# Optimization experiments

Hardware: AMD Instinct MI355X
Metric: run time of the kernel (lower is better)

Reference implementation:

```python
import jax, jax.numpy as jnp
import numpy as np

Ng, Np, B, T = 4096, 512, 128, 100

def setup_inputs() -> dict:
    key = jax.random.key(0)
    ks = jax.random.split(key, 6)
    # xavier-ish scaling for the learned weights
    def xavier(k, shape):
        fan_in, fan_out = shape[1], shape[0]
        lim = jnp.sqrt(6.0 / (fan_in + fan_out))
        return jax.random.uniform(k, shape, jnp.float32, -lim, lim)
    return {
        "v": jax.random.normal(ks[0], (B, T, 2), jnp.float32),
        "p0": jax.random.uniform(ks[1], (B, Np), jnp.float32),
        "W_enc": xavier(ks[2], (Ng, Np)),   # init_position_encoder.weight
        "W_ih": xavier(ks[3], (Ng, 2)),     # RNN weight_ih_l0
        "W_hh": xavier(ks[4], (Ng, Ng)),    # RNN weight_hh_l0
        "W_dec": xavier(ks[5], (Np, Ng)),   # decoder.weight
    }

def reference(v, p0, W_enc, W_ih, W_hh, W_dec):
    # h0 = init_position_encoder(p0): (B, Ng)
    h0 = p0 @ W_enc.T
    # precompute input projections for all steps: (T, B, Ng)
    vin = jnp.einsum('btk,gk->tbg', v, W_ih)

    def step(h, x):
        h_new = jax.nn.relu(x + h @ W_hh.T)  # (B, Ng)
        return h_new, h_new

    _, hs = jax.lax.scan(step, h0, vin)      # hs: (T, B, Ng)
    g = jnp.swapaxes(hs, 0, 1)               # (B, T, Ng)
    preds = g @ W_dec.T                      # (B, T, Np)
    return jax.nn.log_softmax(preds, axis=-1)
```

## Files before the change

### kernel.cpp

```cpp
#include <hip/hip_runtime.h>

#define NG 4096
#define NP 512
#define BSZ 128
#define NT 100

typedef _Float16 f16;
typedef __attribute__((ext_vector_type(8))) _Float16 half8;
typedef __attribute__((ext_vector_type(4))) _Float16 half4v;
typedef __attribute__((ext_vector_type(16))) float f32x16;

__device__ inline f32x16 mfma16(half8 a, half8 b, f32x16 c) {
  return __builtin_amdgcn_mfma_f32_32x32x16_f16(a, b, c, 0, 0, 0);
}
__device__ __forceinline__ void gload16(const void* g, void* l) {
  __builtin_amdgcn_global_load_lds(
      (const __attribute__((address_space(1))) void*)g,
      (__attribute__((address_space(3))) void*)l, 16, 0, 0);
}

__global__ __launch_bounds__(256) void conv_all(
    const float* __restrict__ whh, const float* __restrict__ wdec,
    const float* __restrict__ wenc, const float* __restrict__ p0,
    f16* __restrict__ whh16, f16* __restrict__ wdec16,
    f16* __restrict__ wenc16, f16* __restrict__ p016)
{
  int i = blockIdx.x * 256 + threadIdx.x;
  const float* src; f16* dst; int off;
  if (i < 4194304)      { src = whh;  dst = whh16;  off = 0; }
  else if (i < 4718592) { src = wdec; dst = wdec16; off = 4194304; }
  else if (i < 5242880) { src = wenc; dst = wenc16; off = 4718592; }
  else if (i < 5259264) { src = p0;   dst = p016;   off = 5242880; }
  else return;
  const int j = i - off;
  const float4 x = ((const float4*)src)[j];
  half4v h = { (f16)x.x, (f16)x.y, (f16)x.z, (f16)x.w };
  *(half4v*)&dst[(size_t)j * 4] = h;
}

template<int NS, int KROW>
__global__ __launch_bounds__(256, 2) void gemm_ksplit(
    const f16* __restrict__ bmat, const f16* __restrict__ amat,
    f16* __restrict__ part)
{
  constexpr int NCH = KROW / (NS * 64);
  __shared__ __align__(128) char lds[2 * 32768];
  const int tid = threadIdx.x;
  const int w = tid >> 6, lane = tid & 63;
  const int wm = w & 1, wn = w >> 1;
  const int l31 = lane & 31, hi = lane >> 5;
  const int n0 = blockIdx.y * 128;
  const int k0 = blockIdx.x * (KROW / NS);
  constexpr size_t krb = (size_t)KROW * 2;

  const int lrow8 = lane >> 3;
  const int swz = ((lane & 7) ^ lrow8) * 16;
  const char* gA = (const char*)amat;
  const char* gB = (const char*)bmat + (size_t)n0 * krb;

  f32x16 acc[2][2] = {};

  auto stage = [&](int buf, int c) {
    const size_t kb = (size_t)((k0 + c * 64) * 2) + swz;
    char* lb = lds + buf * 32768;
    #pragma unroll
    for (int j = 0; j < 4; ++j) {
      const int r = w * 32 + j * 8;
      gload16(gA + (size_t)(r + lrow8) * krb + kb, lb + r * 128);
      gload16(gB + (size_t)(r + lrow8) * krb + kb, lb + 16384 + r * 128);
    }
  };
  auto compute = [&](int buf) {
    const char* bA = lds + buf * 32768;
    const char* bB = bA + 16384;
    const int swr = (lane & 7) << 4;
    #pragma unroll
    for (int kk = 0; kk < 4; ++kk) {
      const int bc = (kk * 32 + (hi << 4)) ^ swr;
      half8 a0 = *(const half8*)(bA + (wm * 64 + l31) * 128 + bc);
      half8 a1 = *(const half8*)(bA + (wm * 64 + 32 + l31) * 128 + bc);
      half8 b0 = *(const half8*)(bB + (wn * 64 + l31) * 128 + bc);
      half8 b1 = *(const half8*)(bB + (wn * 64 + 32 + l31) * 128 + bc);
      acc[0][0] = mfma16(a0, b0, acc[0][0]);
      acc[0][1] = mfma16(a0, b1, acc[0][1]);
      acc[1][0] = mfma16(a1, b0, acc[1][0]);
      acc[1][1] = mfma16(a1, b1, acc[1][1]);
    }
  };

  stage(0, 0);
  __syncthreads();
  #pragma unroll 1
  for (int c = 0; c < NCH; ++c) {
    if (c + 1 < NCH) stage((c + 1) & 1, c + 1);
    compute(c & 1);
    __syncthreads();
  }

  f16* po = part + (size_t)blockIdx.x * (BSZ * NG);
  #pragma unroll
  for (int mf = 0; mf < 2; ++mf) {
    #pragma unroll
    for (int q = 0; q < 16; ++q) {
      const int row = wm * 64 + mf * 32 + (q & 3) + 8 * (q >> 2) + 4 * hi;
      #pragma unroll
      for (int nf = 0; nf < 2; ++nf) {
        const int col = n0 + wn * 64 + nf * 32 + l31;
        po[(size_t)row * NG + col] = (f16)acc[mf][nf][q];
      }
    }
  }
}

template<int NS, int DOBIAS>
__global__ __launch_bounds__(256) void reduce_kernel(
    const f16* __restrict__ part, const float* __restrict__ v,
    const float* __restrict__ wih, f16* __restrict__ hout, int t)
{
  const int i = blockIdx.x * 256 + threadIdx.x;
  const int b = i >> 9;
  const int gi = (i & 511) * 8;
  const half8* p = (const half8*)part + (((size_t)b * NG + gi) >> 3);
  float s[8];
  half8 q0 = p[0];
  #pragma unroll
  for (int j = 0; j < 8; ++j) s[j] = (float)q0[j];
  #pragma unroll
  for (int k = 1; k < NS; ++k) {
    half8 q = p[(size_t)k * (BSZ * NG / 8)];
    #pragma unroll
    for (int j = 0; j < 8; ++j) s[j] += (float)q[j];
  }
  half8 h;
  if (DOBIAS) {
    const float2 vb = *(const float2*)&v[((size_t)b * NT + t) * 2];
    const float4* wr = (const float4*)(wih + (size_t)gi * 2);
    #pragma unroll
    for (int j2 = 0; j2 < 4; ++j2) {
      const float4 ww = wr[j2];
      h[j2 * 2]     = (f16)fmaxf(s[j2 * 2]     + vb.x * ww.x + vb.y * ww.y, 0.f);
      h[j2 * 2 + 1] = (f16)fmaxf(s[j2 * 2 + 1] + vb.x * ww.z + vb.y * ww.w, 0.f);
    }
  } else {
    #pragma unroll
    for (int j = 0; j < 8; ++j) h[j] = (f16)s[j];
  }
  *(half8*)&hout[(size_t)b * NG + gi] = h;
}

__global__ __launch_bounds__(512, 2) void decode_kernel(
    const f16* __restrict__ hs, const f16* __restrict__ wdec16,
    float* __restrict__ out)
{
  __shared__ __align__(128) char lds[2 * 73728];
  __shared__ float redm[8][64];
  __shared__ float reds[8][64];
  __shared__ float gLS[64];
  const int tid = threadIdx.x;
  const int w = tid >> 6, lane = tid & 63;
  const int l31 = lane & 31, hi = lane >> 5;
  const int r0 = blockIdx.x * 64;

  const int lrow8 = lane >> 3;
  const int swz = ((lane & 7) ^ lrow8) * 16;
  const char* gA = (const char*)(hs + (size_t)r0 * NG);
  const char* gB = (const char*)wdec16;

  f32x16 acc[2][2] = {};

  auto stage = [&](int buf, int c) {
    const size_t kb = (size_t)(c * 128) + swz;
    char* lb = lds + buf * 73728;
    gload16(gA + (size_t)(w * 8 + lrow8) * (NG * 2) + kb, lb + w * 1024);
    #pragma unroll
    for (int j = 0; j < 8; ++j) {
      const int r = w * 64 + j * 8;
      gload16(gB + (size_t)(r + lrow8) * (NG * 2) + kb, lb + 8192 + r * 128);
    }
  };
  auto compute = [&](int buf) {
    const char* bA = lds + buf * 73728;
    const char* bB = bA + 8192;
    const int swr = (lane & 7) << 4;
    #pragma unroll
    for (int kk = 0; kk < 4; ++kk) {
      const int bc = (kk * 32 + (hi << 4)) ^ swr;
      half8 a0 = *(const half8*)(bA + l31 * 128 + bc);
      half8 a1 = *(const half8*)(bA + (32 + l31) * 128 + bc);
      half8 b0 = *(const half8*)(bB + (w * 64 + l31) * 128 + bc);
      half8 b1 = *(const half8*)(bB + (w * 64 + 32 + l31) * 128 + bc);
      acc[0][0] = mfma16(a0, b0, acc[0][0]);
      acc[0][1] = mfma16(a0, b1, acc[0][1]);
      acc[1][0] = mfma16(a1, b0, acc[1][0]);
      acc[1][1] = mfma16(a1, b1, acc[1][1]);
    }
  };

  stage(0, 0);
  __syncthreads();
  #pragma unroll 1
  for (int c = 0; c < 64; ++c) {
    if (c < 63) stage((c + 1) & 1, c + 1);
    compute(c & 1);
    __syncthreads();
  }

  #pragma unroll
  for (int mf = 0; mf < 2; ++mf) {
    #pragma unroll
    for (int q = 0; q < 16; ++q) {
      float m = fmaxf(acc[mf][0][q], acc[mf][1][q]);
      #pragma unroll
      for (int d = 1; d < 32; d <<= 1) m = fmaxf(m, __shfl_xor(m, d));
      if (l31 == q) redm[w][mf * 32 + (q & 3) + 8 * (q >> 2) + 4 * hi] = m;
    }
  }
  __syncthreads();
  if (tid < 64) {
    float M = redm[0][tid];
    #pragma unroll
    for (int ww = 1; ww < 8; ++ww) M = fmaxf(M, redm[ww][tid]);
    gLS[tid] = M;
  }
  __syncthreads();
  #pragma unroll
  for (int mf = 0; mf < 2; ++mf) {
    #pragma unroll
    for (int q = 0; q < 16; ++q) {
      const int rl = mf * 32 + (q & 3) + 8 * (q >> 2) + 4 * hi;
      const float M = gLS[rl];
      float e = __expf(acc[mf][0][q] - M) + __expf(acc[mf][1][q] - M);
      #pragma unroll
      for (int d = 1; d < 32; d <<= 1) e += __shfl_xor(e, d);
      if (l31 == q) reds[w][rl] = e;
    }
  }
  __syncthreads();
  if (tid < 64) {
    float S = reds[0][tid];
    #pragma unroll
    for (int ww = 1; ww < 8; ++ww) S += reds[ww][tid];
    gLS[tid] = gLS[tid] + __logf(S);
  }
  __syncthreads();
  #pragma unroll
  for (int mf = 0; mf < 2; ++mf) {
    #pragma unroll
    for (int q = 0; q < 16; ++q) {
      const int rl = mf * 32 + (q & 3) + 8 * (q >> 2) + 4 * hi;
      const int r = r0 + rl;
      const int tt = r >> 7, b = r & 127;
      const float lg = gLS[rl];
      float* orow = out + ((size_t)b * NT + tt) * NP + w * 64 + l31;
      orow[0]  = acc[mf][0][q] - lg;
      orow[32] = acc[mf][1][q] - lg;
    }
  }
}


extern "C" void kernel_launch(void* const* d_in, const int* in_sizes, int n_in,
                              void* d_out, int out_size, void* d_ws, size_t ws_size,
                              hipStream_t stream)
{
  const float* v    = (const float*)d_in[0];
  const float* p0   = (const float*)d_in[1];
  const float* wenc = (const float*)d_in[2];
  const float* wih  = (const float*)d_in[3];
  const float* whh  = (const float*)d_in[4];
  const float* wdec = (const float*)d_in[5];
  float* out = (float*)d_out;
  char* ws = (char*)d_ws;

  f16* whh16  = (f16*)(ws);
  f16* wdec16 = (f16*)(ws + 33554432);
  f16* wenc16 = (f16*)(ws + 37748736);
  f16* p016   = (f16*)(ws + 41943040);
  f16* h016   = (f16*)(ws + 42074112);
  f16* hs     = (f16*)(ws + 43122688);
  f16* part   = (f16*)d_out;
  const size_t BNG = (size_t)BSZ * NG;

  conv_all<<<dim3(20544), dim3(256), 0, stream>>>(
      whh, wdec, wenc, p0, whh16, wdec16, wenc16, p016);

  gemm_ksplit<2, 512><<<dim3(2, 32), dim3(256), 0, stream>>>(wenc16, p016, part);
  reduce_kernel<2, 0><<<dim3(256), dim3(256), 0, stream>>>(part, v, wih, h016, 0);

  for (int t = 0; t < NT; ++t) {
    const f16* hp = (t == 0) ? h016 : hs + (size_t)(t - 1) * BNG;
    gemm_ksplit<16, 4096><<<dim3(16, 32), dim3(256), 0, stream>>>(whh16, hp, part);
    reduce_kernel<16, 1><<<dim3(256), dim3(256), 0, stream>>>(part, v, wih, hs + (size_t)t * BNG, t);
  }
  decode_kernel<<<dim3(200), dim3(512), 0, stream>>>(hs, wdec16, out);
}
```

Measured before the change: 1.581 ms.

## Load A operand directly from global into registers, stage only B in LDS

The split-K GEMM kernel no longer stages the A matrix tile through shared memory. Each lane now loads its A fragments straight from global memory into registers, double-buffered across iterations, while only B goes through LDS. This halves LDS usage and removes the A shared-memory reads. In exchange, the A global loads are per-lane and redundant across the waves that share wm, which may cost more global/L2 traffic and more registers.

```diff
diff --git a/kernel.cpp b/kernel.cpp
--- a/kernel.cpp
+++ b/kernel.cpp
@@ -44,7 +44,7 @@
     f16* __restrict__ part)
 {
   constexpr int NCH = KROW / (NS * 64);
-  __shared__ __align__(128) char lds[2 * 32768];
+  __shared__ __align__(128) char lds[2 * 16384];
   const int tid = threadIdx.x;
   const int w = tid >> 6, lane = tid & 63;
   const int wm = w & 1, wn = w >> 1;
@@ -55,45 +55,54 @@
 
   const int lrow8 = lane >> 3;
   const int swz = ((lane & 7) ^ lrow8) * 16;
-  const char* gA = (const char*)amat;
   const char* gB = (const char*)bmat + (size_t)n0 * krb;
+  const f16* pa = amat + (size_t)(wm * 64 + l31) * KROW + k0 + hi * 8;
 
   f32x16 acc[2][2] = {};
+  half8 A0[8], A1[8];
 
   auto stage = [&](int buf, int c) {
     const size_t kb = (size_t)((k0 + c * 64) * 2) + swz;
-    char* lb = lds + buf * 32768;
+    char* lb = lds + buf * 16384;
     #pragma unroll
     for (int j = 0; j < 4; ++j) {
       const int r = w * 32 + j * 8;
-      gload16(gA + (size_t)(r + lrow8) * krb + kb, lb + r * 128);
-      gload16(gB + (size_t)(r + lrow8) * krb + kb, lb + 16384 + r * 128);
-    }
-  };
-  auto compute = [&](int buf) {
-    const char* bA = lds + buf * 32768;
-    const char* bB = bA + 16384;
+      gload16(gB + (size_t)(r + lrow8) * krb + kb, lb + r * 128);
+    }
+  };
+  auto gatherA = [&](half8 (&A)[8], int c) {
+    const f16* p = pa + c * 64;
+    #pragma unroll
+    for (int kk = 0; kk < 4; ++kk) {
+      A[kk]     = *(const half8*)(p + kk * 16);
+      A[kk + 4] = *(const half8*)(p + 32 * KROW + kk * 16);
+    }
+  };
+  auto compute = [&](int buf, half8 (&A)[8]) {
+    const char* bB = lds + buf * 16384;
     const int swr = (lane & 7) << 4;
     #pragma unroll
     for (int kk = 0; kk < 4; ++kk) {
       const int bc = (kk * 32 + (hi << 4)) ^ swr;
-      half8 a0 = *(const half8*)(bA + (wm * 64 + l31) * 128 + bc);
-      half8 a1 = *(const half8*)(bA + (wm * 64 + 32 + l31) * 128 + bc);
       half8 b0 = *(const half8*)(bB + (wn * 64 + l31) * 128 + bc);
       half8 b1 = *(const half8*)(bB + (wn * 64 + 32 + l31) * 128 + bc);
-      acc[0][0] = mfma16(a0, b0, acc[0][0]);
-      acc[0][1] = mfma16(a0, b1, acc[0][1]);
-      acc[1][0] = mfma16(a1, b0, acc[1][0]);
-      acc[1][1] = mfma16(a1, b1, acc[1][1]);
-    }
-  };
-
+      acc[0][0] = mfma16(A[kk],     b0, acc[0][0]);
+      acc[0][1] = mfma16(A[kk],     b1, acc[0][1]);
+      acc[1][0] = mfma16(A[kk + 4], b0, acc[1][0]);
+      acc[1][1] = mfma16(A[kk + 4], b1, acc[1][1]);
+    }
+  };
+
+  gatherA(A0, 0);
   stage(0, 0);
   __syncthreads();
   #pragma unroll 1
-  for (int c = 0; c < NCH; ++c) {
-    if (c + 1 < NCH) stage((c + 1) & 1, c + 1);
-    compute(c & 1);
+  for (int c = 0; c < NCH; c += 2) {
+    if (c + 1 < NCH) { stage(1, c + 1); gatherA(A1, c + 1); }
+    compute(0, A0);
+    __syncthreads();
+    if (c + 2 < NCH) { stage(0, c + 2); gatherA(A0, c + 2); }
+    if (c + 1 < NCH) compute(1, A1);
     __syncthreads();
   }
 
```

Result: slower. 1.973 ms (+24.8%).
